# Kernel optimization log

Hardware: AMD Instinct MI355X
Metric: run time of the kernel (lower is better)

## Reference

```python
import jax, jax.numpy as jnp
import numpy as np

N_SRC, N_DST, N_EDGES = 60000, 50000, 600000
IN_DIM, OUT_DIM = 256, 128


def setup_inputs() -> dict:
    key = jax.random.key(0)
    k1, k2, k3, k4, k5, k6 = jax.random.split(key, 6)
    features = jax.random.normal(k1, (N_SRC, IN_DIM), dtype=jnp.float32)
    t = jax.random.uniform(k2, (N_SRC,), dtype=jnp.float32)
    edge_src = jax.random.randint(k3, (N_EDGES,), 0, N_SRC, dtype=jnp.int32)
    edge_dst = jax.random.randint(k4, (N_EDGES,), 0, N_DST, dtype=jnp.int32)
    # learned params: xavier_normal with relu gain for fc, default for temporal_fc
    gain = float(np.sqrt(2.0))
    std_fc = gain * np.sqrt(2.0 / (IN_DIM + OUT_DIM))
    W_fc = jax.random.normal(k5, (OUT_DIM, IN_DIM), dtype=jnp.float32) * std_fc
    W_t = jax.random.normal(k6, (1, OUT_DIM), dtype=jnp.float32) * (1.0 / np.sqrt(OUT_DIM))
    return {"features": features, "t": t, "edge_src": edge_src,
            "edge_dst": edge_dst, "n_dst": N_DST, "W_fc": W_fc, "W_t": W_t}


def reference(features, t, edge_src, edge_dst, n_dst, W_fc, W_t):
    # z = fc(h), no bias
    z = features @ W_fc.T                      # [n_src, out_dim]
    s = (z @ W_t.T)[:, 0]                      # temporal_fc(z) -> [n_src]
    # edge attention: e = -|t_src - t_dst| (non-differentiable in original)
    e = jax.lax.stop_gradient(-jnp.abs(t[edge_src] - t[edge_dst]))  # [E]
    # mailbox logits: exp(temporal_fc(z_src) * e / 500)
    y = jnp.exp(s[edge_src] * e / 500.0)       # [E]
    # segment softmax over incoming edges of each dst node
    m = jax.ops.segment_max(y, edge_dst, num_segments=n_dst)
    m = jnp.where(jnp.isfinite(m), m, 0.0)     # empty mailboxes
    ex = jnp.exp(y - m[edge_dst])
    denom = jax.ops.segment_sum(ex, edge_dst, num_segments=n_dst)
    alpha = ex / denom[edge_dst]               # [E]
    # weighted neighbor sum
    h = jax.ops.segment_sum(alpha[:, None] * z[edge_src], edge_dst, num_segments=n_dst)
    # residual
    return z[:n_dst] + h
```

## Files before the change

kernel.cpp:

```cpp
#include <hip/hip_runtime.h>
#include <cstdint>

#define NBINS 1024
#define EPB   4096
#define MAXE  1536

typedef __attribute__((ext_vector_type(8))) _Float16 half8;
typedef __attribute__((ext_vector_type(4))) float floatx4;

__global__ __launch_bounds__(256) void convert_w(
    const float* __restrict__ W, _Float16* __restrict__ Wh, int n)
{
    int i = blockIdx.x * 256 + threadIdx.x;
    if (i < n) Wh[i] = (_Float16)W[i];
}

__global__ __launch_bounds__(512, 4) void gemm_mfma(
    const float* __restrict__ A, const _Float16* __restrict__ Wh,
    const float* __restrict__ Wt, _Float16* __restrict__ z16,
    float* __restrict__ s, int M)
{
    __shared__ half8 Wlds[4096];

    const int tid  = threadIdx.x;
    const int lane = tid & 63;
    const int w    = tid >> 6;
    const int m    = lane & 15;
    const int q    = lane >> 4;

#pragma unroll
    for (int it = 0; it < 8; ++it) {
        int pair = w * 8 + it;
        int nt = pair & 7, ks = pair >> 3;
        const _Float16* src = Wh + (size_t)(nt * 16 + m) * 256 + ks * 32 + q * 8;
        Wlds[pair * 64 + lane] = *(const half8*)src;
    }

    const int row_base = blockIdx.x * 128 + w * 16;
    const int arow = min(row_base + m, M - 1);
    const float* ap = A + (size_t)arow * 256 + q * 8;

    float4 abuf[8];
#pragma unroll
    for (int i = 0; i < 4; ++i) {
        abuf[2 * i]     = *(const float4*)(ap + i * 32);
        abuf[2 * i + 1] = *(const float4*)(ap + i * 32 + 4);
    }

    floatx4 acc[8];
#pragma unroll
    for (int nt = 0; nt < 8; ++nt) acc[nt] = (floatx4){0.f, 0.f, 0.f, 0.f};

    __syncthreads();

#pragma unroll
    for (int ks = 0; ks < 8; ++ks) {
        float4 a0 = abuf[(ks & 3) * 2];
        float4 a1 = abuf[(ks & 3) * 2 + 1];
        half8 af;
        af[0] = (_Float16)a0.x; af[1] = (_Float16)a0.y;
        af[2] = (_Float16)a0.z; af[3] = (_Float16)a0.w;
        af[4] = (_Float16)a1.x; af[5] = (_Float16)a1.y;
        af[6] = (_Float16)a1.z; af[7] = (_Float16)a1.w;

        if (ks < 4) {
            abuf[(ks & 3) * 2]     = *(const float4*)(ap + (ks + 4) * 32);
            abuf[(ks & 3) * 2 + 1] = *(const float4*)(ap + (ks + 4) * 32 + 4);
        }

#pragma unroll
        for (int nt = 0; nt < 8; ++nt) {
            half8 bf = Wlds[(ks * 8 + nt) * 64 + lane];
            acc[nt] = __builtin_amdgcn_mfma_f32_16x16x32_f16(
                af, bf, acc[nt], 0, 0, 0);
        }
    }

    float wt[8];
#pragma unroll
    for (int nt = 0; nt < 8; ++nt) wt[nt] = Wt[nt * 16 + m];

    float sp[4] = {0.f, 0.f, 0.f, 0.f};
#pragma unroll
    for (int nt = 0; nt < 8; ++nt)
#pragma unroll
        for (int reg = 0; reg < 4; ++reg)
            sp[reg] += acc[nt][reg] * wt[nt];

#pragma unroll
    for (int reg = 0; reg < 4; ++reg) {
        int row = row_base + q * 4 + reg;
        if (row < M) {
#pragma unroll
            for (int nt = 0; nt < 8; ++nt)
                z16[(size_t)row * 128 + nt * 16 + m] = (_Float16)acc[nt][reg];
        }
    }
#pragma unroll
    for (int off = 1; off <= 8; off <<= 1)
#pragma unroll
        for (int reg = 0; reg < 4; ++reg)
            sp[reg] += __shfl_xor(sp[reg], off, 64);
    if (m == 0) {
#pragma unroll
        for (int reg = 0; reg < 4; ++reg) {
            int row = row_base + q * 4 + reg;
            if (row < M) s[row] = sp[reg];
        }
    }
}

__global__ __launch_bounds__(512) void part_hist(
    const int* __restrict__ edst, int* __restrict__ gcount, int E)
{
    __shared__ int h[NBINS];
    for (int i = threadIdx.x; i < NBINS; i += 512) h[i] = 0;
    __syncthreads();
    int base = blockIdx.x * EPB + threadIdx.x * 8;
    if (base + 8 <= E) {
        int4 d0 = *(const int4*)(edst + base);
        int4 d1 = *(const int4*)(edst + base + 4);
        atomicAdd(&h[d0.x >> 6], 1); atomicAdd(&h[d0.y >> 6], 1);
        atomicAdd(&h[d0.z >> 6], 1); atomicAdd(&h[d0.w >> 6], 1);
        atomicAdd(&h[d1.x >> 6], 1); atomicAdd(&h[d1.y >> 6], 1);
        atomicAdd(&h[d1.z >> 6], 1); atomicAdd(&h[d1.w >> 6], 1);
    } else {
        for (int i = 0; i < 8; ++i)
            if (base + i < E) atomicAdd(&h[edst[base + i] >> 6], 1);
    }
    __syncthreads();
    for (int i = threadIdx.x; i < NBINS; i += 512)
        gcount[blockIdx.x * NBINS + i] = h[i];
}

__global__ __launch_bounds__(256) void part_scanA(
    int* __restrict__ gcount, int* __restrict__ binTot, int NB)
{
    int t = threadIdx.x;
    if (t >= 32) return;
    int b = blockIdx.x * 32 + t;
    int run = 0;
    for (int blk = 0; blk < NB; ++blk) {
        int idx = blk * NBINS + b;
        int c = gcount[idx];
        gcount[idx] = run;
        run += c;
    }
    binTot[b] = run;
}

__global__ __launch_bounds__(1024) void part_scanB(
    const int* __restrict__ binTot, int* __restrict__ binstart)
{
    __shared__ int sb[NBINS];
    int b = threadIdx.x;
    int v = binTot[b];
    sb[b] = v;
    __syncthreads();
    for (int off = 1; off < NBINS; off <<= 1) {
        int add = (b >= off) ? sb[b - off] : 0;
        __syncthreads();
        sb[b] += add;
        __syncthreads();
    }
    binstart[b] = sb[b] - v;
    if (b == NBINS - 1) binstart[NBINS] = sb[b];
}

__global__ __launch_bounds__(512) void part_scatter(
    const int* __restrict__ esrc, const int* __restrict__ edst,
    const float* __restrict__ t, const float* __restrict__ s,
    const int* __restrict__ gcount, const int* __restrict__ binstart,
    int2* __restrict__ part, int E)
{
    __shared__ int h[NBINS];
    for (int i = threadIdx.x; i < NBINS; i += 512)
        h[i] = gcount[blockIdx.x * NBINS + i] + binstart[i];
    __syncthreads();

    int base = blockIdx.x * EPB + threadIdx.x * 8;
    if (base >= E) return;
    int si[8], di[8];
    int nv = E - base; if (nv > 8) nv = 8;
    if (nv == 8) {
        int4 s0 = *(const int4*)(esrc + base);
        int4 s1 = *(const int4*)(esrc + base + 4);
        int4 d0 = *(const int4*)(edst + base);
        int4 d1 = *(const int4*)(edst + base + 4);
        si[0]=s0.x; si[1]=s0.y; si[2]=s0.z; si[3]=s0.w;
        si[4]=s1.x; si[5]=s1.y; si[6]=s1.z; si[7]=s1.w;
        di[0]=d0.x; di[1]=d0.y; di[2]=d0.z; di[3]=d0.w;
        di[4]=d1.x; di[5]=d1.y; di[6]=d1.z; di[7]=d1.w;
    } else {
        for (int i = 0; i < 8; ++i) {
            int e = min(base + i, E - 1);
            si[i] = esrc[e]; di[i] = edst[e];
        }
    }
#pragma unroll
    for (int i = 0; i < 8; ++i) {
        if (i < nv) {
            int pos = atomicAdd(&h[di[i] >> 6], 1);
            float ee = -fabsf(t[si[i]] - t[di[i]]);
            float exv = __expf(__expf(s[si[i]] * ee * (1.0f / 500.0f)));
            part[pos] = make_int2((si[i] & 0xffff) | ((di[i] & 63) << 16),
                                  __float_as_int(exv));
        }
    }
}

__global__ __launch_bounds__(256) void aggregate(
    const _Float16* __restrict__ z16, const int* __restrict__ binstart,
    const int2* __restrict__ part, float* __restrict__ out, int Nd)
{
    __shared__ int2 arr[MAXE];
    __shared__ int lcnt[64];
    __shared__ int loff[65];
    __shared__ int lcur[64];

    const int tid = threadIdx.x;
    const int b = blockIdx.x;
    const int s0 = binstart[b];
    int nE = binstart[b + 1] - s0;
    if (nE > MAXE) nE = MAXE;

    if (tid < 64) lcnt[tid] = 0;
    __syncthreads();
    for (int i = tid; i < nE; i += 256)
        atomicAdd(&lcnt[(part[s0 + i].x >> 16) & 63], 1);
    __syncthreads();
    if (tid < 64) {
        int v = lcnt[tid], x = v;
#pragma unroll
        for (int off = 1; off < 64; off <<= 1) {
            int n = __shfl_up(x, off, 64);
            if (tid >= off) x += n;
        }
        loff[tid + 1] = x;
        lcur[tid] = x - v;
        if (tid == 0) loff[0] = 0;
    }
    __syncthreads();
    for (int i = tid; i < nE; i += 256) {
        int2 r = part[s0 + i];
        int pos = atomicAdd(&lcur[(r.x >> 16) & 63], 1);
        arr[pos] = r;
    }
    __syncthreads();

    const int lane = tid & 63;
    const int w = tid >> 6;
    const int g = lane >> 3;
    const int c = lane & 7;

#pragma unroll
    for (int k = 0; k < 2; ++k) {
        int loc = w * 16 + k * 8 + g;
        int d = b * 64 + loc;
        if (d >= Nd) continue;
        int jb = loff[loc], je = loff[loc + 1];

        float acc[16];
#pragma unroll
        for (int i = 0; i < 16; ++i) acc[i] = 0.f;
        float dsum = 0.f;

        int j = jb;
        for (; j + 1 < je; j += 2) {
            int2 r0 = arr[j];
            int2 r1 = arr[j + 1];
            float x0 = __int_as_float(r0.y);
            float x1 = __int_as_float(r1.y);
            const half8* zp0 = (const half8*)(z16 + (size_t)(r0.x & 0xffff) * 128 + c * 16);
            const half8* zp1 = (const half8*)(z16 + (size_t)(r1.x & 0xffff) * 128 + c * 16);
            half8 a0 = zp0[0], a1 = zp0[1];
            half8 b0 = zp1[0], b1 = zp1[1];
            dsum += x0 + x1;
#pragma unroll
            for (int i = 0; i < 8; ++i) {
                acc[i]     = fmaf(x0, (float)a0[i], acc[i]);
                acc[8 + i] = fmaf(x0, (float)a1[i], acc[8 + i]);
                acc[i]     = fmaf(x1, (float)b0[i], acc[i]);
                acc[8 + i] = fmaf(x1, (float)b1[i], acc[8 + i]);
            }
        }
        if (j < je) {
            int2 r0 = arr[j];
            float x0 = __int_as_float(r0.y);
            const half8* zp0 = (const half8*)(z16 + (size_t)(r0.x & 0xffff) * 128 + c * 16);
            half8 a0 = zp0[0], a1 = zp0[1];
            dsum += x0;
#pragma unroll
            for (int i = 0; i < 8; ++i) {
                acc[i]     = fmaf(x0, (float)a0[i], acc[i]);
                acc[8 + i] = fmaf(x0, (float)a1[i], acc[8 + i]);
            }
        }

        float inv = (je > jb) ? 1.0f / dsum : 0.0f;
        const half8* zr = (const half8*)(z16 + (size_t)d * 128 + c * 16);
        half8 r0 = zr[0], r1 = zr[1];
        float* op = out + (size_t)d * 128 + c * 16;
        *(float4*)(op + 0)  = make_float4(fmaf(acc[0],  inv, (float)r0[0]),
                                          fmaf(acc[1],  inv, (float)r0[1]),
                                          fmaf(acc[2],  inv, (float)r0[2]),
                                          fmaf(acc[3],  inv, (float)r0[3]));
        *(float4*)(op + 4)  = make_float4(fmaf(acc[4],  inv, (float)r0[4]),
                                          fmaf(acc[5],  inv, (float)r0[5]),
                                          fmaf(acc[6],  inv, (float)r0[6]),
                                          fmaf(acc[7],  inv, (float)r0[7]));
        *(float4*)(op + 8)  = make_float4(fmaf(acc[8],  inv, (float)r1[0]),
                                          fmaf(acc[9],  inv, (float)r1[1]),
                                          fmaf(acc[10], inv, (float)r1[2]),
                                          fmaf(acc[11], inv, (float)r1[3]));
        *(float4*)(op + 12) = make_float4(fmaf(acc[12], inv, (float)r1[4]),
                                          fmaf(acc[13], inv, (float)r1[5]),
                                          fmaf(acc[14], inv, (float)r1[6]),
                                          fmaf(acc[15], inv, (float)r1[7]));
    }
}

extern "C" void kernel_launch(void* const* d_in, const int* in_sizes, int n_in,
                              void* d_out, int out_size, void* d_ws, size_t ws_size,
                              hipStream_t stream)
{
    const float* features = (const float*)d_in[0];
    const float* t        = (const float*)d_in[1];
    const int*   esrc     = (const int*)d_in[2];
    const int*   edst     = (const int*)d_in[3];
    const float* Wfc      = (const float*)d_in[5];
    const float* Wt       = (const float*)d_in[6];
    float* out = (float*)d_out;

    const int M  = in_sizes[1];
    const int E  = in_sizes[2];
    const int OD = in_sizes[6];
    const int Nd = out_size / OD;
    const int ID = in_sizes[5] / OD;

    const int NB = (E + EPB - 1) / EPB;

    _Float16* z16   = (_Float16*)d_ws;
    float*    s     = (float*)(z16 + (size_t)M * 128);
    _Float16* Wh    = (_Float16*)(s + M);
    int*      gcount = (int*)(Wh + (size_t)OD * ID);
    int*      binTot = gcount + (size_t)NB * NBINS;
    int*      binstart = binTot + NBINS;
    int2*     part  = (int2*)(binstart + NBINS + 4);

    convert_w<<<(OD * ID + 255) / 256, 256, 0, stream>>>(Wfc, Wh, OD * ID);
    part_hist<<<NB, 512, 0, stream>>>(edst, gcount, E);
    part_scanA<<<NBINS / 32, 256, 0, stream>>>(gcount, binTot, NB);
    part_scanB<<<1, 1024, 0, stream>>>(binTot, binstart);
    gemm_mfma<<<(M + 127) / 128, 512, 0, stream>>>(features, Wh, Wt, z16, s, M);
    part_scatter<<<NB, 512, 0, stream>>>(esrc, edst, t, s, gcount, binstart,
                                         part, E);
    aggregate<<<(Nd + 63) / 64, 256, 0, stream>>>(z16, binstart, part, out, Nd);
}
```

Before: 205.6 us.

## Fuse weight conversion into GEMM, parallelize bin scan, overlap scatter atomics

Removes the separate convert_w launch by converting the fp32 weights to fp16 while staging them into LDS inside the GEMM. The per-bin column scan now uses one wavefront per bin with a shuffle-based prefix scan instead of one serial thread per bin. part_scatter computes local ranks with LDS atomics before the global base load, so that load overlaps the atomic work. aggregate keeps its records in registers so the partition is read from global memory only once. Each GEMM block now converts the weights itself, which is redundant work, and aggregate's register caching assumes MAXE/256 is at most 6.

```diff
diff --git a/kernel.cpp b/kernel.cpp
--- a/kernel.cpp
+++ b/kernel.cpp
@@ -8,15 +8,8 @@
 typedef __attribute__((ext_vector_type(8))) _Float16 half8;
 typedef __attribute__((ext_vector_type(4))) float floatx4;
 
-__global__ __launch_bounds__(256) void convert_w(
-    const float* __restrict__ W, _Float16* __restrict__ Wh, int n)
-{
-    int i = blockIdx.x * 256 + threadIdx.x;
-    if (i < n) Wh[i] = (_Float16)W[i];
-}
-
 __global__ __launch_bounds__(512, 4) void gemm_mfma(
-    const float* __restrict__ A, const _Float16* __restrict__ Wh,
+    const float* __restrict__ A, const float* __restrict__ W,
     const float* __restrict__ Wt, _Float16* __restrict__ z16,
     float* __restrict__ s, int M)
 {
@@ -32,8 +25,15 @@
     for (int it = 0; it < 8; ++it) {
         int pair = w * 8 + it;
         int nt = pair & 7, ks = pair >> 3;
-        const _Float16* src = Wh + (size_t)(nt * 16 + m) * 256 + ks * 32 + q * 8;
-        Wlds[pair * 64 + lane] = *(const half8*)src;
+        const float* src = W + (size_t)(nt * 16 + m) * 256 + ks * 32 + q * 8;
+        float4 w0 = *(const float4*)src;
+        float4 w1 = *(const float4*)(src + 4);
+        half8 h;
+        h[0] = (_Float16)w0.x; h[1] = (_Float16)w0.y;
+        h[2] = (_Float16)w0.z; h[3] = (_Float16)w0.w;
+        h[4] = (_Float16)w1.x; h[5] = (_Float16)w1.y;
+        h[6] = (_Float16)w1.z; h[7] = (_Float16)w1.w;
+        Wlds[pair * 64 + lane] = h;
     }
 
     const int row_base = blockIdx.x * 128 + w * 16;
@@ -133,20 +133,27 @@
         gcount[blockIdx.x * NBINS + i] = h[i];
 }
 
-__global__ __launch_bounds__(256) void part_scanA(
+__global__ __launch_bounds__(256) void part_scan(
     int* __restrict__ gcount, int* __restrict__ binTot, int NB)
 {
-    int t = threadIdx.x;
-    if (t >= 32) return;
-    int b = blockIdx.x * 32 + t;
+    int b    = blockIdx.x * 4 + (threadIdx.x >> 6);
+    int lane = threadIdx.x & 63;
+    if (b >= NBINS) return;
+    int chunks = (NB + 63) >> 6;
     int run = 0;
-    for (int blk = 0; blk < NB; ++blk) {
-        int idx = blk * NBINS + b;
-        int c = gcount[idx];
-        gcount[idx] = run;
-        run += c;
-    }
-    binTot[b] = run;
+    for (int c = 0; c < chunks; ++c) {
+        int blk = c * 64 + lane;
+        int v = (blk < NB) ? gcount[(size_t)blk * NBINS + b] : 0;
+        int incl = v;
+#pragma unroll
+        for (int off = 1; off < 64; off <<= 1) {
+            int n = __shfl_up(incl, off, 64);
+            if (lane >= off) incl += n;
+        }
+        if (blk < NB) gcount[(size_t)blk * NBINS + b] = run + incl - v;
+        run += __shfl(incl, 63, 64);
+    }
+    if (lane == 0) binTot[b] = run;
 }
 
 __global__ __launch_bounds__(1024) void part_scanB(
@@ -173,38 +180,48 @@
     const int* __restrict__ gcount, const int* __restrict__ binstart,
     int2* __restrict__ part, int E)
 {
-    __shared__ int h[NBINS];
+    __shared__ int hloc[NBINS];
+    __shared__ int hbase[NBINS];
+    for (int i = threadIdx.x; i < NBINS; i += 512) hloc[i] = 0;
+    __syncthreads();
+
+    int base = blockIdx.x * EPB + threadIdx.x * 8;
+    int si[8], di[8], rk[8];
+    int nv = 0;
+    if (base < E) {
+        nv = E - base; if (nv > 8) nv = 8;
+        if (nv == 8) {
+            int4 s0 = *(const int4*)(esrc + base);
+            int4 s1 = *(const int4*)(esrc + base + 4);
+            int4 d0 = *(const int4*)(edst + base);
+            int4 d1 = *(const int4*)(edst + base + 4);
+            si[0]=s0.x; si[1]=s0.y; si[2]=s0.z; si[3]=s0.w;
+            si[4]=s1.x; si[5]=s1.y; si[6]=s1.z; si[7]=s1.w;
+            di[0]=d0.x; di[1]=d0.y; di[2]=d0.z; di[3]=d0.w;
+            di[4]=d1.x; di[5]=d1.y; di[6]=d1.z; di[7]=d1.w;
+        } else {
+            for (int i = 0; i < 8; ++i) {
+                int e = min(base + i, E - 1);
+                si[i] = esrc[e]; di[i] = edst[e];
+            }
+        }
+#pragma unroll
+        for (int i = 0; i < 8; ++i)
+            if (i < nv) rk[i] = atomicAdd(&hloc[di[i] >> 6], 1);
+    }
+
     for (int i = threadIdx.x; i < NBINS; i += 512)
-        h[i] = gcount[blockIdx.x * NBINS + i] + binstart[i];
-    __syncthreads();
-
-    int base = blockIdx.x * EPB + threadIdx.x * 8;
-    if (base >= E) return;
-    int si[8], di[8];
-    int nv = E - base; if (nv > 8) nv = 8;
-    if (nv == 8) {
-        int4 s0 = *(const int4*)(esrc + base);
-        int4 s1 = *(const int4*)(esrc + base + 4);
-        int4 d0 = *(const int4*)(edst + base);
-        int4 d1 = *(const int4*)(edst + base + 4);
-        si[0]=s0.x; si[1]=s0.y; si[2]=s0.z; si[3]=s0.w;
-        si[4]=s1.x; si[5]=s1.y; si[6]=s1.z; si[7]=s1.w;
-        di[0]=d0.x; di[1]=d0.y; di[2]=d0.z; di[3]=d0.w;
-        di[4]=d1.x; di[5]=d1.y; di[6]=d1.z; di[7]=d1.w;
-    } else {
-        for (int i = 0; i < 8; ++i) {
-            int e = min(base + i, E - 1);
-            si[i] = esrc[e]; di[i] = edst[e];
-        }
-    }
+        hbase[i] = binstart[i] + gcount[(size_t)blockIdx.x * NBINS + i];
+    __syncthreads();
+
 #pragma unroll
     for (int i = 0; i < 8; ++i) {
         if (i < nv) {
-            int pos = atomicAdd(&h[di[i] >> 6], 1);
             float ee = -fabsf(t[si[i]] - t[di[i]]);
             float exv = __expf(__expf(s[si[i]] * ee * (1.0f / 500.0f)));
-            part[pos] = make_int2((si[i] & 0xffff) | ((di[i] & 63) << 16),
-                                  __float_as_int(exv));
+            part[hbase[di[i] >> 6] + rk[i]] =
+                make_int2((si[i] & 0xffff) | ((di[i] & 63) << 16),
+                          __float_as_int(exv));
         }
     }
 }
@@ -216,7 +233,6 @@
     __shared__ int2 arr[MAXE];
     __shared__ int lcnt[64];
     __shared__ int loff[65];
-    __shared__ int lcur[64];
 
     const int tid = threadIdx.x;
     const int b = blockIdx.x;
@@ -226,8 +242,16 @@
 
     if (tid < 64) lcnt[tid] = 0;
     __syncthreads();
-    for (int i = tid; i < nE; i += 256)
-        atomicAdd(&lcnt[(part[s0 + i].x >> 16) & 63], 1);
+
+    int2 rec[6]; int rrk[6], rloc[6], nrec = 0;
+    for (int i = tid; i < nE; i += 256) {
+        int2 r = part[s0 + i];
+        int loc = (r.x >> 16) & 63;
+        rec[nrec] = r;
+        rloc[nrec] = loc;
+        rrk[nrec] = atomicAdd(&lcnt[loc], 1);
+        ++nrec;
+    }
     __syncthreads();
     if (tid < 64) {
         int v = lcnt[tid], x = v;
@@ -237,15 +261,11 @@
             if (tid >= off) x += n;
         }
         loff[tid + 1] = x;
-        lcur[tid] = x - v;
         if (tid == 0) loff[0] = 0;
     }
     __syncthreads();
-    for (int i = tid; i < nE; i += 256) {
-        int2 r = part[s0 + i];
-        int pos = atomicAdd(&lcur[(r.x >> 16) & 63], 1);
-        arr[pos] = r;
-    }
+    for (int i = 0; i < nrec; ++i)
+        arr[loff[rloc[i]] + rrk[i]] = rec[i];
     __syncthreads();
 
     const int lane = tid & 63;
@@ -336,23 +356,20 @@
     const int E  = in_sizes[2];
     const int OD = in_sizes[6];
     const int Nd = out_size / OD;
-    const int ID = in_sizes[5] / OD;
 
     const int NB = (E + EPB - 1) / EPB;
 
-    _Float16* z16   = (_Float16*)d_ws;
-    float*    s     = (float*)(z16 + (size_t)M * 128);
-    _Float16* Wh    = (_Float16*)(s + M);
-    int*      gcount = (int*)(Wh + (size_t)OD * ID);
-    int*      binTot = gcount + (size_t)NB * NBINS;
+    _Float16* z16      = (_Float16*)d_ws;
+    float*    s        = (float*)(z16 + (size_t)M * 128);
+    int*      gcount   = (int*)(s + M);
+    int*      binTot   = gcount + (size_t)NB * NBINS;
     int*      binstart = binTot + NBINS;
-    int2*     part  = (int2*)(binstart + NBINS + 4);
-
-    convert_w<<<(OD * ID + 255) / 256, 256, 0, stream>>>(Wfc, Wh, OD * ID);
+    int2*     part     = (int2*)(binstart + NBINS + 4);
+
     part_hist<<<NB, 512, 0, stream>>>(edst, gcount, E);
-    part_scanA<<<NBINS / 32, 256, 0, stream>>>(gcount, binTot, NB);
+    part_scan<<<NBINS / 4, 256, 0, stream>>>(gcount, binTot, NB);
     part_scanB<<<1, 1024, 0, stream>>>(binTot, binstart);
-    gemm_mfma<<<(M + 127) / 128, 512, 0, stream>>>(features, Wh, Wt, z16, s, M);
+    gemm_mfma<<<(M + 127) / 128, 512, 0, stream>>>(features, Wfc, Wt, z16, s, M);
     part_scatter<<<NB, 512, 0, stream>>>(esrc, edst, t, s, gcount, binstart,
                                          part, E);
     aggregate<<<(Nd + 63) / 64, 256, 0, stream>>>(z16, binstart, part, out, Nd);
```

Result: faster. 179.1 us (-12.9%).
